# Performance work log

Measured on AMD Instinct MI355X. Metric: run time of the kernel, lower is better.

Reference implementation:

```python
import jax, jax.numpy as jnp
import numpy as np

N_EMB = 1024
EMB_DIM = 256
COMMITMENT_COST = 0.25


def setup_inputs() -> dict:
    key = jax.random.key(0)
    k1, k2 = jax.random.split(key)
    B = 65536
    x = jax.random.normal(k1, (B, EMB_DIM), dtype=jnp.float32)
    init_bound = 1.0 / 512
    embedding = jax.random.uniform(k2, (N_EMB, EMB_DIM), dtype=jnp.float32,
                                   minval=-init_bound, maxval=init_bound)
    return {"x": x, "embedding": embedding}


def reference(x, embedding):
    B, D = x.shape
    M = embedding.shape[0]
    x_flat = jax.lax.stop_gradient(x)
    # distances[b,m] = ||x_b||^2 + ||e_m||^2 - 2 x_b . e_m  (torch.addmm form)
    distances = (jnp.sum(embedding ** 2, axis=1)[None, :]
                 + jnp.sum(x_flat ** 2, axis=1, keepdims=True)
                 - 2.0 * x_flat @ embedding.T)
    indices = jnp.argmin(distances.astype(jnp.float32), axis=-1)  # [B] int
    quantized = embedding[indices]  # [B, D]

    # commitment loss (quantized detached), masked by non-padding rows
    e_latent = jnp.mean((x - jax.lax.stop_gradient(quantized)) ** 2, axis=-1)  # [B]
    nonpadding = (jnp.sum(jnp.abs(x), axis=-1) > 0).astype(x.dtype)
    loss = COMMITMENT_COST * jnp.sum(e_latent * nonpadding) / jnp.sum(nonpadding)

    # straight-through estimator
    quantized_st = x + jax.lax.stop_gradient(quantized - x)

    # perplexity: avg one-hot probs via bincount (scatter-add, no BxM one-hot)
    counts = jnp.zeros((M,), dtype=jnp.float32).at[indices].add(1.0)
    avg_probs = counts / B
    perplexity = jnp.exp(-jnp.sum(avg_probs * jnp.log(avg_probs + 1e-10)))

    return quantized_st, loss, indices, perplexity
```

## Files before the change

kernel.cpp:

```cpp
#include <hip/hip_runtime.h>

#define BROWS 65536
#define DDIM 256
#define MCODES 1024
#define FLAG_MARGIN 3e-4f
#define RGRP 16

typedef __attribute__((ext_vector_type(8))) _Float16 h8f16;
typedef __attribute__((ext_vector_type(4))) float float4v;

__device__ inline unsigned short f2h_bits(float f) {
  union { _Float16 h; unsigned short u; } cv;
  cv.h = (_Float16)f;
  return cv.u;
}

__global__ __launch_bounds__(256)
void prep_kernel(const float* __restrict__ x, const float* __restrict__ emb,
                 float* __restrict__ xnorm, float* __restrict__ enorm,
                 float* __restrict__ counts, int* __restrict__ nflag,
                 float* __restrict__ loss_extra,
                 unsigned short* __restrict__ eimg, float* __restrict__ embT) {
  int b = blockIdx.x;
  int tid = threadIdx.x;
  if (b < 4160) {
    int t = b * 256 + tid;
    if (t < MCODES) counts[t] = 0.0f;
    if (t == 0) *nflag = 0;
    if (t < 2) loss_extra[t] = 0.0f;
    int row = t >> 4;
    int lane = t & 15;
    const float* p;
    float* dst;
    int r;
    if (row < BROWS) { p = x + (size_t)row * DDIM; dst = xnorm; r = row; }
    else             { p = emb + (size_t)(row - BROWS) * DDIM; dst = enorm; r = row - BROWS; }
    int half = (lane >> 3) & 1;
    int j = lane & 7;
    const float* q = p + half * 128 + j;
    float v = q[0];
    float acc = __fmul_rn(v, v);
    #pragma unroll
    for (int i = 1; i < 16; ++i) {
      v = q[i * 8];
      acc = __fadd_rn(acc, __fmul_rn(v, v));
    }
    float o;
    o = __shfl_xor(acc, 1, 64); acc = __fadd_rn(acc, o);
    o = __shfl_xor(acc, 2, 64); acc = __fadd_rn(acc, o);
    o = __shfl_xor(acc, 4, 64); acc = __fadd_rn(acc, o);
    o = __shfl_xor(acc, 8, 64); acc = __fadd_rn(acc, o);
    if (lane == 0) dst[r] = acc;
  } else if (b < 4288) {
    int t = (b - 4160) * 256 + tid;
    int lane = t & 63;
    int tile = (t >> 6) & 1;
    int kstep = (t >> 7) & 7;
    int cc = t >> 10;
    int code = cc * 32 + tile * 16 + (lane & 15);
    int kb = kstep * 32 + (lane >> 4) * 8;
    const float* src = emb + (size_t)code * DDIM + kb;
    union { unsigned short u[8]; uint4 v; } out;
    #pragma unroll
    for (int jj = 0; jj < 8; ++jj) out.u[jj] = f2h_bits(src[jj] * 256.0f);
    ((uint4*)eimg)[t] = out.v;
  } else {
    int t = (b - 4288) * 256 + tid;
    int base = t * 4;
    int k = base >> 10;
    int m = base & 1023;
    float4 v;
    v.x = emb[(size_t)(m + 0) * DDIM + k];
    v.y = emb[(size_t)(m + 1) * DDIM + k];
    v.z = emb[(size_t)(m + 2) * DDIM + k];
    v.w = emb[(size_t)(m + 3) * DDIM + k];
    *(float4*)&embT[base] = v;
  }
}

__global__ __launch_bounds__(256, 4)
void score_kernel(const float* __restrict__ x, const float* __restrict__ emb,
                  const float* __restrict__ enorm_g,
                  const unsigned short* __restrict__ eimg,
                  int* __restrict__ idx_out, float* __restrict__ out_idxf,
                  float* __restrict__ qout, float* __restrict__ counts,
                  float* __restrict__ wred, float* __restrict__ npred,
                  int* __restrict__ nflag, int* __restrict__ flist) {
  __shared__ __align__(16) unsigned short ebuf[2][8192];
  __shared__ float enorm_s[MCODES];
  __shared__ int lcount;
  __shared__ int lbase;
  __shared__ int lrows[64];
  __shared__ int sidx[64];
  __shared__ unsigned char sflag[64];

  int tid = threadIdx.x;
  int w = tid >> 6;
  int lane = tid & 63;
  int quad = lane >> 4;
  int rowBase = blockIdx.x * 64;
  int waveRow = rowBase + w * 16;

  if (tid == 0) lcount = 0;
  for (int i = tid; i < MCODES; i += 256) enorm_s[i] = enorm_g[i];

  h8f16 xh[8];
  const float* xbase = x + (size_t)(waveRow + (lane & 15)) * DDIM + quad * 8;
  #pragma unroll
  for (int ks = 0; ks < 8; ++ks) {
    const float4* p = (const float4*)(xbase + ks * 32);
    float4 v0 = p[0], v1 = p[1];
    h8f16 h;
    h[0] = (_Float16)v0.x; h[1] = (_Float16)v0.y;
    h[2] = (_Float16)v0.z; h[3] = (_Float16)v0.w;
    h[4] = (_Float16)v1.x; h[5] = (_Float16)v1.y;
    h[6] = (_Float16)v1.z; h[7] = (_Float16)v1.w;
    xh[ks] = h;
  }

  float b1[4], b2[4];
  int i1[4];
  #pragma unroll
  for (int reg = 0; reg < 4; ++reg) { b1[reg] = 3.4e38f; b2[reg] = 3.4e38f; i1[reg] = 0; }

  #define STAGE_CC(ccv, bf) do { \
    const unsigned short* g_ = eimg + (size_t)(ccv) * 8192 + w * 2048 + lane * 8; \
    unsigned short* l_ = &ebuf[(bf)][w * 2048]; \
    _Pragma("unroll") \
    for (int j_ = 0; j_ < 4; ++j_) { \
      __builtin_amdgcn_global_load_lds((const __attribute__((address_space(1))) unsigned int*)(g_ + j_ * 512), \
                                       (__attribute__((address_space(3))) unsigned int*)(l_ + j_ * 512), 16, 0, 0); \
    } \
  } while (0)

  STAGE_CC(0, 0);

  for (int cc = 0; cc < 32; ++cc) {
    int buf = cc & 1;
    __syncthreads();
    if (cc < 31) STAGE_CC(cc + 1, buf ^ 1);

    float4v acc0 = (float4v){0.f, 0.f, 0.f, 0.f};
    float4v acc1 = (float4v){0.f, 0.f, 0.f, 0.f};
    #pragma unroll
    for (int ks = 0; ks < 8; ++ks) {
      h8f16 e0 = *(const h8f16*)&ebuf[buf][ks * 1024 + lane * 8];
      h8f16 e1 = *(const h8f16*)&ebuf[buf][ks * 1024 + 512 + lane * 8];
      acc0 = __builtin_amdgcn_mfma_f32_16x16x32_f16(xh[ks], e0, acc0, 0, 0, 0);
      acc1 = __builtin_amdgcn_mfma_f32_16x16x32_f16(xh[ks], e1, acc1, 0, 0, 0);
    }

    #pragma unroll
    for (int t2 = 0; t2 < 2; ++t2) {
      int m = cc * 32 + t2 * 16 + (lane & 15);
      float en = enorm_s[m];
      #pragma unroll
      for (int reg = 0; reg < 4; ++reg) {
        float av = t2 ? acc1[reg] : acc0[reg];
        float s = __fadd_rn(en, __fmul_rn(-0.0078125f, av));
        if (s < b1[reg]) { b2[reg] = b1[reg]; b1[reg] = s; i1[reg] = m; }
        else { b2[reg] = fminf(b2[reg], s); }
      }
    }
  }

  #pragma unroll
  for (int off = 1; off < 16; off <<= 1) {
    #pragma unroll
    for (int reg = 0; reg < 4; ++reg) {
      float ob1 = __shfl_xor(b1[reg], off, 64);
      float ob2 = __shfl_xor(b2[reg], off, 64);
      int oi = __shfl_xor(i1[reg], off, 64);
      float cb1 = b1[reg], cb2 = b2[reg];
      int ci = i1[reg];
      float nb1, nb2; int ni;
      if (ob1 < cb1)      { nb1 = ob1; ni = oi; nb2 = fminf(cb1, ob2); }
      else if (cb1 < ob1) { nb1 = cb1; ni = ci; nb2 = fminf(ob1, cb2); }
      else                { nb1 = cb1; ni = min(ci, oi); nb2 = cb1; }
      b1[reg] = nb1; b2[reg] = nb2; i1[reg] = ni;
    }
  }

  if ((lane & 15) == 0) {
    #pragma unroll
    for (int reg = 0; reg < 4; ++reg) {
      int row = waveRow + quad * 4 + reg;
      int bi = i1[reg];
      idx_out[row] = bi;
      out_idxf[row] = (float)bi;
      int lr = row - rowBase;
      sidx[lr] = bi;
      int fl = (__fadd_rn(b2[reg], -b1[reg]) <= FLAG_MARGIN) ? 1 : 0;
      sflag[lr] = (unsigned char)fl;
      if (fl) {
        int pp = atomicAdd(&lcount, 1);
        lrows[pp] = row;
      }
    }
  }
  __syncthreads();
  if (tid == 0 && lcount > 0) lbase = atomicAdd(nflag, lcount);
  __syncthreads();
  if (tid < lcount) flist[lbase + tid] = lrows[tid];

  if (w < 2) {
    float lsum = 0.0f, nsum = 0.0f;
    for (int it = 0; it < 32; ++it) {
      int lr = w * 32 + it;
      int row = rowBase + lr;
      int id = sidx[lr];
      int fl = sflag[lr];
      float4 xv = ((const float4*)x)[(size_t)row * 64 + lane];
      float4 ev = ((const float4*)emb)[(size_t)id * 64 + lane];
      float4 q;
      q.x = __fadd_rn(xv.x, __fadd_rn(ev.x, -xv.x));
      q.y = __fadd_rn(xv.y, __fadd_rn(ev.y, -xv.y));
      q.z = __fadd_rn(xv.z, __fadd_rn(ev.z, -xv.z));
      q.w = __fadd_rn(xv.w, __fadd_rn(ev.w, -xv.w));
      ((float4*)qout)[(size_t)row * 64 + lane] = q;

      float d0 = xv.x - ev.x, d1 = xv.y - ev.y, d2 = xv.z - ev.z, d3 = xv.w - ev.w;
      float loc = d0 * d0 + d1 * d1 + d2 * d2 + d3 * d3;
      float la = fabsf(xv.x) + fabsf(xv.y) + fabsf(xv.z) + fabsf(xv.w);
      #pragma unroll
      for (int off = 32; off > 0; off >>= 1) {
        loc += __shfl_xor(loc, off, 64);
        la += __shfl_xor(la, off, 64);
      }
      if (lane == 0 && !fl) {
        float np = (la > 0.0f) ? 1.0f : 0.0f;
        lsum += (loc * (1.0f / 256.0f)) * np;
        nsum += np;
        atomicAdd(&counts[id], 1.0f);
      }
    }
    if (lane == 0) {
      wred[blockIdx.x * 2 + w] = lsum;
      npred[blockIdx.x * 2 + w] = nsum;
    }
  }
  #undef STAGE_CC
}

__global__ __launch_bounds__(256)
void rescore_kernel(const float* __restrict__ x, const float* __restrict__ emb,
                    const float* __restrict__ embT,
                    const float* __restrict__ xnorm, const float* __restrict__ enorm,
                    int* __restrict__ idx_out, float* __restrict__ out_idxf,
                    float* __restrict__ qout, float* __restrict__ counts,
                    float* __restrict__ loss_extra,
                    const int* __restrict__ nflag, const int* __restrict__ flist) {
  __shared__ float xs[RGRP][DDIM];
  __shared__ float xnr[RGRP];
  __shared__ int rown[RGRP];
  __shared__ int sbf[RGRP];
  __shared__ float rv[RGRP][256];
  __shared__ int ri[RGRP][256];
  int tid = threadIdx.x;
  int n = nflag[0];

  for (int g = blockIdx.x; g * RGRP < n; g += 1024) {
    int base = g * RGRP;
    int cnt = min(RGRP, n - base);
    __syncthreads();
    if (tid < RGRP) {
      int rr = flist[base + min(tid, cnt - 1)];
      rown[tid] = rr;
      xnr[tid] = xnorm[rr];
    }
    __syncthreads();
    #pragma unroll
    for (int r = 0; r < RGRP; ++r) xs[r][tid] = x[(size_t)rown[r] * DDIM + tid];
    __syncthreads();

    float d[4][RGRP];
    #pragma unroll
    for (int c4 = 0; c4 < 4; ++c4)
      #pragma unroll
      for (int r = 0; r < RGRP; ++r) d[c4][r] = 0.0f;

    float e_cur[4][4], e_nxt[4][4];
    #pragma unroll
    for (int kk = 0; kk < 4; ++kk)
      #pragma unroll
      for (int c4 = 0; c4 < 4; ++c4)
        e_cur[kk][c4] = embT[(size_t)kk * 1024 + c4 * 256 + tid];

    for (int k0 = 0; k0 < DDIM; k0 += 4) {
      if (k0 + 4 < DDIM) {
        #pragma unroll
        for (int kk = 0; kk < 4; ++kk)
          #pragma unroll
          for (int c4 = 0; c4 < 4; ++c4)
            e_nxt[kk][c4] = embT[(size_t)(k0 + 4 + kk) * 1024 + c4 * 256 + tid];
      }
      #pragma unroll
      for (int r = 0; r < RGRP; ++r) {
        float4 xv = *(const float4*)&xs[r][k0];
        #pragma unroll
        for (int c4 = 0; c4 < 4; ++c4) {
          d[c4][r] = fmaf(xv.x, e_cur[0][c4], d[c4][r]);
          d[c4][r] = fmaf(xv.y, e_cur[1][c4], d[c4][r]);
          d[c4][r] = fmaf(xv.z, e_cur[2][c4], d[c4][r]);
          d[c4][r] = fmaf(xv.w, e_cur[3][c4], d[c4][r]);
        }
      }
      #pragma unroll
      for (int kk = 0; kk < 4; ++kk)
        #pragma unroll
        for (int c4 = 0; c4 < 4; ++c4)
          e_cur[kk][c4] = e_nxt[kk][c4];
    }

    float b[RGRP]; int bi[RGRP];
    #pragma unroll
    for (int r = 0; r < RGRP; ++r) { b[r] = 3.4e38f; bi[r] = 0; }
    #pragma unroll
    for (int c4 = 0; c4 < 4; ++c4) {
      int m = c4 * 256 + tid;
      float en = enorm[m];
      #pragma unroll
      for (int r = 0; r < RGRP; ++r) {
        float T = __fadd_rn(en, xnr[r]);
        float s = __fadd_rn(T, __fmul_rn(-2.0f, d[c4][r]));
        if (s < b[r] || (s == b[r] && m < bi[r])) { b[r] = s; bi[r] = m; }
      }
    }
    #pragma unroll
    for (int r = 0; r < RGRP; ++r) { rv[r][tid] = b[r]; ri[r][tid] = bi[r]; }
    __syncthreads();
    for (int st = 128; st > 0; st >>= 1) {
      if (tid < st) {
        #pragma unroll
        for (int r = 0; r < RGRP; ++r) {
          float v = rv[r][tid + st]; int m2 = ri[r][tid + st];
          if (v < rv[r][tid] || (v == rv[r][tid] && m2 < ri[r][tid])) { rv[r][tid] = v; ri[r][tid] = m2; }
        }
      }
      __syncthreads();
    }

    if (tid < RGRP) sbf[tid] = ri[tid][0];
    __syncthreads();

    float* laf = (float*)ri;
    #pragma unroll
    for (int r = 0; r < RGRP; ++r) {
      int bf = sbf[r];
      float xv = xs[r][tid];
      float ev = emb[(size_t)bf * DDIM + tid];
      if (r < cnt) {
        float q = __fadd_rn(xv, __fadd_rn(ev, -xv));
        qout[(size_t)rown[r] * DDIM + tid] = q;
      }
      float dd = xv - ev;
      rv[r][tid] = dd * dd;
      laf[r * 256 + tid] = fabsf(xv);
    }
    __syncthreads();
    for (int st = 128; st > 0; st >>= 1) {
      if (tid < st) {
        #pragma unroll
        for (int r = 0; r < RGRP; ++r) {
          rv[r][tid] += rv[r][tid + st];
          laf[r * 256 + tid] += laf[r * 256 + tid + st];
        }
      }
      __syncthreads();
    }
    if (tid < cnt) {
      int bfin = sbf[tid];
      int row = rown[tid];
      float np = (laf[tid * 256] > 0.0f) ? 1.0f : 0.0f;
      atomicAdd(&loss_extra[0], (rv[tid][0] * (1.0f / 256.0f)) * np);
      atomicAdd(&loss_extra[1], np);
      atomicAdd(&counts[bfin], 1.0f);
      idx_out[row] = bfin;
      out_idxf[row] = (float)bfin;
    }
  }
}

__global__ __launch_bounds__(256)
void finalize_kernel(const float* __restrict__ counts,
                     const float* __restrict__ wred, const float* __restrict__ npred,
                     const float* __restrict__ loss_extra,
                     float* __restrict__ out_loss, float* __restrict__ out_perp) {
  __shared__ float red[768];
  int t = threadIdx.x;
  float esum = 0.0f, lsum = 0.0f, nsum = 0.0f;
  for (int m = t; m < MCODES; m += 256) {
    float p = counts[m] * (1.0f / 65536.0f);
    esum += p * logf(p + 1e-10f);
  }
  for (int i = t; i < 512; i += 256) {
    lsum += (wred[4 * i] + wred[4 * i + 1]) + (wred[4 * i + 2] + wred[4 * i + 3]);
    nsum += (npred[4 * i] + npred[4 * i + 1]) + (npred[4 * i + 2] + npred[4 * i + 3]);
  }
  red[t] = esum; red[256 + t] = lsum; red[512 + t] = nsum;
  __syncthreads();
  for (int s = 128; s > 0; s >>= 1) {
    if (t < s) {
      red[t] += red[t + s];
      red[256 + t] += red[256 + t + s];
      red[512 + t] += red[512 + t + s];
    }
    __syncthreads();
  }
  if (t == 0) {
    *out_perp = expf(-red[0]);
    float ls = red[256] + loss_extra[0];
    float ns = red[512] + loss_extra[1];
    *out_loss = 0.25f * ls / ns;
  }
}

extern "C" void kernel_launch(void* const* d_in, const int* in_sizes, int n_in,
                              void* d_out, int out_size, void* d_ws, size_t ws_size,
                              hipStream_t stream) {
  (void)in_sizes; (void)n_in; (void)out_size; (void)ws_size;
  const float* x = (const float*)d_in[0];
  const float* emb = (const float*)d_in[1];

  float* out = (float*)d_out;
  float* qst = out;
  float* out_loss = out + 16777216;
  float* out_idxf = out + 16777217;
  float* out_perp = out + 16842753;

  float* ws = (float*)d_ws;
  float* xnorm = ws;
  float* enorm = ws + 65536;
  int* idx = (int*)(ws + 66560);
  float* counts = ws + 132096;
  float* wred = ws + 133120;
  float* npred = ws + 135168;
  float* loss_extra = ws + 137216;
  int* nflag = (int*)(ws + 137218);
  int* flist = (int*)(ws + 137220);
  unsigned short* eimg = (unsigned short*)(ws + 202756);
  float* embT = ws + 333828;

  prep_kernel<<<4544, 256, 0, stream>>>(x, emb, xnorm, enorm, counts, nflag, loss_extra, eimg, embT);
  score_kernel<<<1024, 256, 0, stream>>>(x, emb, enorm, eimg, idx, out_idxf,
                                         qst, counts, wred, npred, nflag, flist);
  rescore_kernel<<<1024, 256, 0, stream>>>(x, emb, embT, xnorm, enorm, idx, out_idxf,
                                           qst, counts, loss_extra, nflag, flist);
  finalize_kernel<<<1, 256, 0, stream>>>(counts, wred, npred, loss_extra, out_loss, out_perp);
}
```

Measured before the change: 252.2 us.

## Double rows per score block and compute x norms only for flagged rows

The score kernel now handles 128 rows per block, with each wave covering 32 rows across two MFMA row groups. Every codebook tile staged in LDS is therefore reused for twice as many rows, and the grid is halved. The prep kernel no longer reads all of x to compute row norms. The rescore kernel instead computes norms only for the flagged rows it loads into shared memory. The costs are higher register pressure (launch bounds lowered to 2 blocks per CU), fewer blocks for latency hiding, and all four waves now doing the quantize/loss epilogue.

```diff
diff --git a/kernel.cpp b/kernel.cpp
--- a/kernel.cpp
+++ b/kernel.cpp
@@ -5,6 +5,7 @@
 #define MCODES 1024
 #define FLAG_MARGIN 3e-4f
 #define RGRP 16
+#define NPART 512
 
 typedef __attribute__((ext_vector_type(8))) _Float16 h8f16;
 typedef __attribute__((ext_vector_type(4))) float float4v;
@@ -16,25 +17,21 @@
 }
 
 __global__ __launch_bounds__(256)
-void prep_kernel(const float* __restrict__ x, const float* __restrict__ emb,
-                 float* __restrict__ xnorm, float* __restrict__ enorm,
+void prep_kernel(const float* __restrict__ emb,
+                 float* __restrict__ enorm,
                  float* __restrict__ counts, int* __restrict__ nflag,
                  float* __restrict__ loss_extra,
                  unsigned short* __restrict__ eimg, float* __restrict__ embT) {
   int b = blockIdx.x;
   int tid = threadIdx.x;
-  if (b < 4160) {
+  if (b < 64) {
     int t = b * 256 + tid;
     if (t < MCODES) counts[t] = 0.0f;
     if (t == 0) *nflag = 0;
     if (t < 2) loss_extra[t] = 0.0f;
     int row = t >> 4;
     int lane = t & 15;
-    const float* p;
-    float* dst;
-    int r;
-    if (row < BROWS) { p = x + (size_t)row * DDIM; dst = xnorm; r = row; }
-    else             { p = emb + (size_t)(row - BROWS) * DDIM; dst = enorm; r = row - BROWS; }
+    const float* p = emb + (size_t)row * DDIM;
     int half = (lane >> 3) & 1;
     int j = lane & 7;
     const float* q = p + half * 128 + j;
@@ -50,9 +47,9 @@
     o = __shfl_xor(acc, 2, 64); acc = __fadd_rn(acc, o);
     o = __shfl_xor(acc, 4, 64); acc = __fadd_rn(acc, o);
     o = __shfl_xor(acc, 8, 64); acc = __fadd_rn(acc, o);
-    if (lane == 0) dst[r] = acc;
-  } else if (b < 4288) {
-    int t = (b - 4160) * 256 + tid;
+    if (lane == 0) enorm[row] = acc;
+  } else if (b < 192) {
+    int t = (b - 64) * 256 + tid;
     int lane = t & 63;
     int tile = (t >> 6) & 1;
     int kstep = (t >> 7) & 7;
@@ -65,7 +62,7 @@
     for (int jj = 0; jj < 8; ++jj) out.u[jj] = f2h_bits(src[jj] * 256.0f);
     ((uint4*)eimg)[t] = out.v;
   } else {
-    int t = (b - 4288) * 256 + tid;
+    int t = (b - 192) * 256 + tid;
     int base = t * 4;
     int k = base >> 10;
     int m = base & 1023;
@@ -78,50 +75,56 @@
   }
 }
 
-__global__ __launch_bounds__(256, 4)
+__global__ __launch_bounds__(256, 2)
 void score_kernel(const float* __restrict__ x, const float* __restrict__ emb,
                   const float* __restrict__ enorm_g,
                   const unsigned short* __restrict__ eimg,
                   int* __restrict__ idx_out, float* __restrict__ out_idxf,
                   float* __restrict__ qout, float* __restrict__ counts,
-                  float* __restrict__ wred, float* __restrict__ npred,
+                  float* __restrict__ loss_part, float* __restrict__ np_part,
                   int* __restrict__ nflag, int* __restrict__ flist) {
   __shared__ __align__(16) unsigned short ebuf[2][8192];
   __shared__ float enorm_s[MCODES];
   __shared__ int lcount;
   __shared__ int lbase;
-  __shared__ int lrows[64];
-  __shared__ int sidx[64];
-  __shared__ unsigned char sflag[64];
+  __shared__ int lrows[128];
+  __shared__ int sidx[128];
+  __shared__ unsigned char sflag[128];
+  __shared__ float red[8];
 
   int tid = threadIdx.x;
   int w = tid >> 6;
   int lane = tid & 63;
   int quad = lane >> 4;
-  int rowBase = blockIdx.x * 64;
-  int waveRow = rowBase + w * 16;
+  int rowBase = blockIdx.x * 128;
+  int waveRow = rowBase + w * 32;
 
   if (tid == 0) lcount = 0;
   for (int i = tid; i < MCODES; i += 256) enorm_s[i] = enorm_g[i];
 
-  h8f16 xh[8];
+  h8f16 xh[2][8];
   const float* xbase = x + (size_t)(waveRow + (lane & 15)) * DDIM + quad * 8;
   #pragma unroll
-  for (int ks = 0; ks < 8; ++ks) {
-    const float4* p = (const float4*)(xbase + ks * 32);
-    float4 v0 = p[0], v1 = p[1];
-    h8f16 h;
-    h[0] = (_Float16)v0.x; h[1] = (_Float16)v0.y;
-    h[2] = (_Float16)v0.z; h[3] = (_Float16)v0.w;
-    h[4] = (_Float16)v1.x; h[5] = (_Float16)v1.y;
-    h[6] = (_Float16)v1.z; h[7] = (_Float16)v1.w;
-    xh[ks] = h;
-  }
-
-  float b1[4], b2[4];
-  int i1[4];
+  for (int rg = 0; rg < 2; ++rg) {
+    #pragma unroll
+    for (int ks = 0; ks < 8; ++ks) {
+      const float4* p = (const float4*)(xbase + rg * 16 * DDIM + ks * 32);
+      float4 v0 = p[0], v1 = p[1];
+      h8f16 h;
+      h[0] = (_Float16)v0.x; h[1] = (_Float16)v0.y;
+      h[2] = (_Float16)v0.z; h[3] = (_Float16)v0.w;
+      h[4] = (_Float16)v1.x; h[5] = (_Float16)v1.y;
+      h[6] = (_Float16)v1.z; h[7] = (_Float16)v1.w;
+      xh[rg][ks] = h;
+    }
+  }
+
+  float b1[2][4], b2[2][4];
+  int i1[2][4];
   #pragma unroll
-  for (int reg = 0; reg < 4; ++reg) { b1[reg] = 3.4e38f; b2[reg] = 3.4e38f; i1[reg] = 0; }
+  for (int rg = 0; rg < 2; ++rg)
+    #pragma unroll
+    for (int reg = 0; reg < 4; ++reg) { b1[rg][reg] = 3.4e38f; b2[rg][reg] = 3.4e38f; i1[rg][reg] = 0; }
 
   #define STAGE_CC(ccv, bf) do { \
     const unsigned short* g_ = eimg + (size_t)(ccv) * 8192 + w * 2048 + lane * 8; \
@@ -140,14 +143,21 @@
     __syncthreads();
     if (cc < 31) STAGE_CC(cc + 1, buf ^ 1);
 
-    float4v acc0 = (float4v){0.f, 0.f, 0.f, 0.f};
-    float4v acc1 = (float4v){0.f, 0.f, 0.f, 0.f};
+    float4v acc[2][2];
+    #pragma unroll
+    for (int rg = 0; rg < 2; ++rg)
+      #pragma unroll
+      for (int t2 = 0; t2 < 2; ++t2) acc[rg][t2] = (float4v){0.f, 0.f, 0.f, 0.f};
+
     #pragma unroll
     for (int ks = 0; ks < 8; ++ks) {
       h8f16 e0 = *(const h8f16*)&ebuf[buf][ks * 1024 + lane * 8];
       h8f16 e1 = *(const h8f16*)&ebuf[buf][ks * 1024 + 512 + lane * 8];
-      acc0 = __builtin_amdgcn_mfma_f32_16x16x32_f16(xh[ks], e0, acc0, 0, 0, 0);
-      acc1 = __builtin_amdgcn_mfma_f32_16x16x32_f16(xh[ks], e1, acc1, 0, 0, 0);
+      #pragma unroll
+      for (int rg = 0; rg < 2; ++rg) {
+        acc[rg][0] = __builtin_amdgcn_mfma_f32_16x16x32_f16(xh[rg][ks], e0, acc[rg][0], 0, 0, 0);
+        acc[rg][1] = __builtin_amdgcn_mfma_f32_16x16x32_f16(xh[rg][ks], e1, acc[rg][1], 0, 0, 0);
+      }
     }
 
     #pragma unroll
@@ -155,89 +165,94 @@
       int m = cc * 32 + t2 * 16 + (lane & 15);
       float en = enorm_s[m];
       #pragma unroll
-      for (int reg = 0; reg < 4; ++reg) {
-        float av = t2 ? acc1[reg] : acc0[reg];
-        float s = __fadd_rn(en, __fmul_rn(-0.0078125f, av));
-        if (s < b1[reg]) { b2[reg] = b1[reg]; b1[reg] = s; i1[reg] = m; }
-        else { b2[reg] = fminf(b2[reg], s); }
-      }
+      for (int rg = 0; rg < 2; ++rg)
+        #pragma unroll
+        for (int reg = 0; reg < 4; ++reg) {
+          float s = __fadd_rn(en, __fmul_rn(-0.0078125f, acc[rg][t2][reg]));
+          if (s < b1[rg][reg]) { b2[rg][reg] = b1[rg][reg]; b1[rg][reg] = s; i1[rg][reg] = m; }
+          else { b2[rg][reg] = fminf(b2[rg][reg], s); }
+        }
     }
   }
 
   #pragma unroll
   for (int off = 1; off < 16; off <<= 1) {
     #pragma unroll
-    for (int reg = 0; reg < 4; ++reg) {
-      float ob1 = __shfl_xor(b1[reg], off, 64);
-      float ob2 = __shfl_xor(b2[reg], off, 64);
-      int oi = __shfl_xor(i1[reg], off, 64);
-      float cb1 = b1[reg], cb2 = b2[reg];
-      int ci = i1[reg];
-      float nb1, nb2; int ni;
-      if (ob1 < cb1)      { nb1 = ob1; ni = oi; nb2 = fminf(cb1, ob2); }
-      else if (cb1 < ob1) { nb1 = cb1; ni = ci; nb2 = fminf(ob1, cb2); }
-      else                { nb1 = cb1; ni = min(ci, oi); nb2 = cb1; }
-      b1[reg] = nb1; b2[reg] = nb2; i1[reg] = ni;
-    }
+    for (int rg = 0; rg < 2; ++rg)
+      #pragma unroll
+      for (int reg = 0; reg < 4; ++reg) {
+        float ob1 = __shfl_xor(b1[rg][reg], off, 64);
+        float ob2 = __shfl_xor(b2[rg][reg], off, 64);
+        int oi = __shfl_xor(i1[rg][reg], off, 64);
+        float cb1 = b1[rg][reg], cb2 = b2[rg][reg];
+        int ci = i1[rg][reg];
+        float nb1, nb2; int ni;
+        if (ob1 < cb1)      { nb1 = ob1; ni = oi; nb2 = fminf(cb1, ob2); }
+        else if (cb1 < ob1) { nb1 = cb1; ni = ci; nb2 = fminf(ob1, cb2); }
+        else                { nb1 = cb1; ni = min(ci, oi); nb2 = cb1; }
+        b1[rg][reg] = nb1; b2[rg][reg] = nb2; i1[rg][reg] = ni;
+      }
   }
 
   if ((lane & 15) == 0) {
     #pragma unroll
-    for (int reg = 0; reg < 4; ++reg) {
-      int row = waveRow + quad * 4 + reg;
-      int bi = i1[reg];
-      idx_out[row] = bi;
-      out_idxf[row] = (float)bi;
-      int lr = row - rowBase;
-      sidx[lr] = bi;
-      int fl = (__fadd_rn(b2[reg], -b1[reg]) <= FLAG_MARGIN) ? 1 : 0;
-      sflag[lr] = (unsigned char)fl;
-      if (fl) {
-        int pp = atomicAdd(&lcount, 1);
-        lrows[pp] = row;
-      }
-    }
+    for (int rg = 0; rg < 2; ++rg)
+      #pragma unroll
+      for (int reg = 0; reg < 4; ++reg) {
+        int row = waveRow + rg * 16 + quad * 4 + reg;
+        int bi = i1[rg][reg];
+        idx_out[row] = bi;
+        out_idxf[row] = (float)bi;
+        int lr = row - rowBase;
+        sidx[lr] = bi;
+        int fl = (__fadd_rn(b2[rg][reg], -b1[rg][reg]) <= FLAG_MARGIN) ? 1 : 0;
+        sflag[lr] = (unsigned char)fl;
+        if (fl) {
+          int pp = atomicAdd(&lcount, 1);
+          lrows[pp] = row;
+        }
+      }
   }
   __syncthreads();
   if (tid == 0 && lcount > 0) lbase = atomicAdd(nflag, lcount);
   __syncthreads();
   if (tid < lcount) flist[lbase + tid] = lrows[tid];
 
-  if (w < 2) {
-    float lsum = 0.0f, nsum = 0.0f;
-    for (int it = 0; it < 32; ++it) {
-      int lr = w * 32 + it;
-      int row = rowBase + lr;
-      int id = sidx[lr];
-      int fl = sflag[lr];
-      float4 xv = ((const float4*)x)[(size_t)row * 64 + lane];
-      float4 ev = ((const float4*)emb)[(size_t)id * 64 + lane];
-      float4 q;
-      q.x = __fadd_rn(xv.x, __fadd_rn(ev.x, -xv.x));
-      q.y = __fadd_rn(xv.y, __fadd_rn(ev.y, -xv.y));
-      q.z = __fadd_rn(xv.z, __fadd_rn(ev.z, -xv.z));
-      q.w = __fadd_rn(xv.w, __fadd_rn(ev.w, -xv.w));
-      ((float4*)qout)[(size_t)row * 64 + lane] = q;
-
-      float d0 = xv.x - ev.x, d1 = xv.y - ev.y, d2 = xv.z - ev.z, d3 = xv.w - ev.w;
-      float loc = d0 * d0 + d1 * d1 + d2 * d2 + d3 * d3;
-      float la = fabsf(xv.x) + fabsf(xv.y) + fabsf(xv.z) + fabsf(xv.w);
-      #pragma unroll
-      for (int off = 32; off > 0; off >>= 1) {
-        loc += __shfl_xor(loc, off, 64);
-        la += __shfl_xor(la, off, 64);
-      }
-      if (lane == 0 && !fl) {
-        float np = (la > 0.0f) ? 1.0f : 0.0f;
-        lsum += (loc * (1.0f / 256.0f)) * np;
-        nsum += np;
-        atomicAdd(&counts[id], 1.0f);
-      }
-    }
-    if (lane == 0) {
-      wred[blockIdx.x * 2 + w] = lsum;
-      npred[blockIdx.x * 2 + w] = nsum;
-    }
+  float lsum = 0.0f, nsum = 0.0f;
+  for (int it = 0; it < 32; ++it) {
+    int lr = w * 32 + it;
+    int row = rowBase + lr;
+    int id = sidx[lr];
+    int fl = sflag[lr];
+    float4 xv = ((const float4*)x)[(size_t)row * 64 + lane];
+    float4 ev = ((const float4*)emb)[(size_t)id * 64 + lane];
+    float4 q;
+    q.x = __fadd_rn(xv.x, __fadd_rn(ev.x, -xv.x));
+    q.y = __fadd_rn(xv.y, __fadd_rn(ev.y, -xv.y));
+    q.z = __fadd_rn(xv.z, __fadd_rn(ev.z, -xv.z));
+    q.w = __fadd_rn(xv.w, __fadd_rn(ev.w, -xv.w));
+    ((float4*)qout)[(size_t)row * 64 + lane] = q;
+
+    float d0 = xv.x - ev.x, d1 = xv.y - ev.y, d2 = xv.z - ev.z, d3 = xv.w - ev.w;
+    float loc = d0 * d0 + d1 * d1 + d2 * d2 + d3 * d3;
+    float la = fabsf(xv.x) + fabsf(xv.y) + fabsf(xv.z) + fabsf(xv.w);
+    #pragma unroll
+    for (int off = 32; off > 0; off >>= 1) {
+      loc += __shfl_xor(loc, off, 64);
+      la += __shfl_xor(la, off, 64);
+    }
+    if (lane == 0 && !fl) {
+      float np = (la > 0.0f) ? 1.0f : 0.0f;
+      lsum += (loc * (1.0f / 256.0f)) * np;
+      nsum += np;
+      atomicAdd(&counts[id], 1.0f);
+    }
+  }
+  if (lane == 0) { red[w] = lsum; red[4 + w] = nsum; }
+  __syncthreads();
+  if (tid == 0) {
+    loss_part[blockIdx.x] = (red[0] + red[1]) + (red[2] + red[3]);
+    np_part[blockIdx.x] = (red[4] + red[5]) + (red[6] + red[7]);
   }
   #undef STAGE_CC
 }
@@ -245,7 +260,7 @@
 __global__ __launch_bounds__(256)
 void rescore_kernel(const float* __restrict__ x, const float* __restrict__ emb,
                     const float* __restrict__ embT,
-                    const float* __restrict__ xnorm, const float* __restrict__ enorm,
+                    const float* __restrict__ enorm,
                     int* __restrict__ idx_out, float* __restrict__ out_idxf,
                     float* __restrict__ qout, float* __restrict__ counts,
                     float* __restrict__ loss_extra,
@@ -266,11 +281,32 @@
     if (tid < RGRP) {
       int rr = flist[base + min(tid, cnt - 1)];
       rown[tid] = rr;
-      xnr[tid] = xnorm[rr];
     }
     __syncthreads();
     #pragma unroll
     for (int r = 0; r < RGRP; ++r) xs[r][tid] = x[(size_t)rown[r] * DDIM + tid];
+    __syncthreads();
+
+    {
+      int r = tid >> 4;
+      int lane = tid & 15;
+      int half = (lane >> 3) & 1;
+      int j = lane & 7;
+      const float* q = &xs[r][half * 128 + j];
+      float v = q[0];
+      float acc = __fmul_rn(v, v);
+      #pragma unroll
+      for (int i = 1; i < 16; ++i) {
+        v = q[i * 8];
+        acc = __fadd_rn(acc, __fmul_rn(v, v));
+      }
+      float o;
+      o = __shfl_xor(acc, 1, 64); acc = __fadd_rn(acc, o);
+      o = __shfl_xor(acc, 2, 64); acc = __fadd_rn(acc, o);
+      o = __shfl_xor(acc, 4, 64); acc = __fadd_rn(acc, o);
+      o = __shfl_xor(acc, 8, 64); acc = __fadd_rn(acc, o);
+      if (lane == 0) xnr[r] = acc;
+    }
     __syncthreads();
 
     float d[4][RGRP];
@@ -383,7 +419,7 @@
 
 __global__ __launch_bounds__(256)
 void finalize_kernel(const float* __restrict__ counts,
-                     const float* __restrict__ wred, const float* __restrict__ npred,
+                     const float* __restrict__ loss_part, const float* __restrict__ np_part,
                      const float* __restrict__ loss_extra,
                      float* __restrict__ out_loss, float* __restrict__ out_perp) {
   __shared__ float red[768];
@@ -393,9 +429,9 @@
     float p = counts[m] * (1.0f / 65536.0f);
     esum += p * logf(p + 1e-10f);
   }
-  for (int i = t; i < 512; i += 256) {
-    lsum += (wred[4 * i] + wred[4 * i + 1]) + (wred[4 * i + 2] + wred[4 * i + 3]);
-    nsum += (npred[4 * i] + npred[4 * i + 1]) + (npred[4 * i + 2] + npred[4 * i + 3]);
+  for (int i = t; i < NPART; i += 256) {
+    lsum += loss_part[i];
+    nsum += np_part[i];
   }
   red[t] = esum; red[256 + t] = lsum; red[512 + t] = nsum;
   __syncthreads();
@@ -429,22 +465,21 @@
   float* out_perp = out + 16842753;
 
   float* ws = (float*)d_ws;
-  float* xnorm = ws;
-  float* enorm = ws + 65536;
-  int* idx = (int*)(ws + 66560);
-  float* counts = ws + 132096;
-  float* wred = ws + 133120;
-  float* npred = ws + 135168;
-  float* loss_extra = ws + 137216;
-  int* nflag = (int*)(ws + 137218);
-  int* flist = (int*)(ws + 137220);
-  unsigned short* eimg = (unsigned short*)(ws + 202756);
-  float* embT = ws + 333828;
-
-  prep_kernel<<<4544, 256, 0, stream>>>(x, emb, xnorm, enorm, counts, nflag, loss_extra, eimg, embT);
-  score_kernel<<<1024, 256, 0, stream>>>(x, emb, enorm, eimg, idx, out_idxf,
-                                         qst, counts, wred, npred, nflag, flist);
-  rescore_kernel<<<1024, 256, 0, stream>>>(x, emb, embT, xnorm, enorm, idx, out_idxf,
+  float* enorm = ws;
+  int* idx = (int*)(ws + 1024);
+  float* counts = ws + 66560;
+  float* lpart = ws + 67584;
+  float* npart = ws + 68096;
+  float* loss_extra = ws + 68608;
+  int* nflag = (int*)(ws + 68610);
+  int* flist = (int*)(ws + 68612);
+  unsigned short* eimg = (unsigned short*)(ws + 134160);
+  float* embT = ws + 265232;
+
+  prep_kernel<<<448, 256, 0, stream>>>(emb, enorm, counts, nflag, loss_extra, eimg, embT);
+  score_kernel<<<512, 256, 0, stream>>>(x, emb, enorm, eimg, idx, out_idxf,
+                                        qst, counts, lpart, npart, nflag, flist);
+  rescore_kernel<<<1024, 256, 0, stream>>>(x, emb, embT, enorm, idx, out_idxf,
                                            qst, counts, loss_extra, nflag, flist);
-  finalize_kernel<<<1, 256, 0, stream>>>(counts, wred, npred, loss_extra, out_loss, out_perp);
-}
+  finalize_kernel<<<1, 256, 0, stream>>>(counts, lpart, npart, loss_extra, out_loss, out_perp);
+}
```

Measured after the change: 247.1 us. 1.02x faster.
